# Kernel tuning notes

Hardware: AMD Instinct MI355X
Metric: run time of the kernel (lower is better)

Reference implementation:

```python
import jax, jax.numpy as jnp
import numpy as np

NUM_VERTS = 6890
NUM_FACES = 13776
MAX_COLLISIONS = 8      # BVH(max_collisions=8)
SIGMA = 0.5             # df_cone_height
POINT2PLANE = False
PENALIZE_OUTSIDE = True
COLL_LOSS_WEIGHT = 1.0
EPS = 1e-8


def setup_inputs() -> dict:
    key = jax.random.key(0)
    k1, k2 = jax.random.split(key)
    vertices = jax.random.normal(k1, (1, NUM_VERTS, 3), dtype=jnp.float32)
    # flat face index list, as consumed by index_select(vertices, 1, faces)
    faces = jax.random.randint(k2, (NUM_FACES * 3,), 0, NUM_VERTS, dtype=jnp.int32)
    return {"vertices": vertices, "faces": faces}


def _find_collisions(triangles, faces_mat):
    """Fixed-shape emulation of the BVH broad phase.

    triangles: [B,F,3,3]. Returns collision_idxs [B, F*K, 2] int32 with -1 padding,
    pairs (receiver, intruder) whose AABBs overlap, excluding pairs of triangles
    that share a vertex (as the BVH does; this also removes self-pairs).
    """
    B, F = triangles.shape[0], triangles.shape[1]
    bbmin = triangles.min(axis=2)   # [B,F,3]
    bbmax = triangles.max(axis=2)   # [B,F,3]
    overlap = jnp.ones((B, F, F), dtype=bool)
    for a in range(3):  # fixed 3-axis loop
        lo = bbmin[:, :, a]
        hi = bbmax[:, :, a]
        overlap = overlap & (lo[:, :, None] <= hi[:, None, :]) & (lo[:, None, :] <= hi[:, :, None])
    # triangles sharing any vertex are never reported as collisions
    share = jnp.zeros((F, F), dtype=bool)
    for a in range(3):
        for b in range(3):
            share = share | (faces_mat[:, a][:, None] == faces_mat[:, b][None, :])
    valid = overlap & ~share[None]
    vals, idxs = jax.lax.top_k(valid.astype(jnp.float32), MAX_COLLISIONS)  # [B,F,K]
    intr = jnp.where(vals > 0, idxs, -1)
    recv = jnp.broadcast_to(jnp.arange(F, dtype=jnp.int32)[None, :, None], intr.shape)
    recv = jnp.where(intr >= 0, recv, -1)
    return jnp.stack([recv.reshape(B, -1), intr.reshape(B, -1)], axis=-1)  # [B,F*K,2]


def _cone_field_penalty(src_tri, pts):
    """Conical distance-field penalty (Tzionas et al.) of src triangles
    evaluated at the 3 vertices of the paired triangle.
    src_tri: [B,P,3,3] field-generating triangles; pts: [B,P,3,3] query vertices.
    Returns per-pair penalty [B,P].
    """
    e0 = src_tri[..., 1, :] - src_tri[..., 0, :]
    e1 = src_tri[..., 2, :] - src_tri[..., 0, :]
    n = jnp.cross(e0, e1)
    n = n / (jnp.linalg.norm(n, axis=-1, keepdims=True) + EPS)  # unit normal
    c = src_tri.mean(axis=-2)                                    # triangle center
    u = pts - c[..., None, :]                                    # [B,P,3,3]
    h = jnp.sum(u * n[..., None, :], axis=-1)                    # signed height [B,P,3]
    r = jnp.linalg.norm(u - h[..., None] * n[..., None, :], axis=-1)  # radial dist
    radial = jax.nn.relu(1.0 - r / SIGMA)        # linear falloff of the cone
    depth = jax.nn.relu(-h)                      # penetration depth behind the face
    if PENALIZE_OUTSIDE:
        depth = depth + jax.nn.relu(h) * jnp.exp(-h / SIGMA)  # soft outside penalty
    phi = radial * depth
    per_v = radial * h * h if POINT2PLANE else phi * phi
    return per_v.sum(axis=-1)  # sum over the 3 query vertices -> [B,P]


def reference(vertices, faces):
    B = vertices.shape[0]
    triangles = vertices[:, faces, :].reshape(B, -1, 3, 3)  # [B,F,3,3]
    faces_mat = faces.reshape(-1, 3)
    # collision search runs under no_grad in the original
    coll = _find_collisions(jax.lax.stop_gradient(triangles), faces_mat)  # [B,P,2]
    valid = (coll[..., 0] >= 0)
    recv_idx = jnp.maximum(coll[..., 0], 0)
    intr_idx = jnp.maximum(coll[..., 1], 0)
    bi = jnp.arange(B)[:, None]
    recv_tri = triangles[bi, recv_idx]  # [B,P,3,3]
    intr_tri = triangles[bi, intr_idx]  # [B,P,3,3]
    pen = _cone_field_penalty(recv_tri, intr_tri) + _cone_field_penalty(intr_tri, recv_tri)
    return COLL_LOSS_WEIGHT * jnp.sum(jnp.where(valid, pen, 0.0))
```

## Files before the change

kernel.cpp:

```cpp
#include <hip/hip_runtime.h>

#define NF   13776
#define NFP  13824
#define KMAX 8
#define EPS  1e-8f
#define CBLK 2048

__global__ __launch_bounds__(256) void prep_kernel(
    const float* __restrict__ verts,
    const int*   __restrict__ faces,
    float4* __restrict__ tri,
    float4* __restrict__ lo4, float4* __restrict__ hi4,
    int* __restrict__ f2)
{
    int f = blockIdx.x * blockDim.x + threadIdx.x;
    if (f >= NFP) return;
    if (f >= NF) {
        lo4[f] = make_float4(INFINITY, INFINITY, INFINITY, __int_as_float(-1));
        hi4[f] = make_float4(-INFINITY, -INFINITY, -INFINITY, __int_as_float(-1));
        f2[f]  = -1;
        return;
    }
    int ia = faces[3 * f + 0], ib = faces[3 * f + 1], ic = faces[3 * f + 2];
    float ax = verts[3 * ia + 0], ay = verts[3 * ia + 1], az = verts[3 * ia + 2];
    float bx = verts[3 * ib + 0], by = verts[3 * ib + 1], bz = verts[3 * ib + 2];
    float cx = verts[3 * ic + 0], cy = verts[3 * ic + 1], cz = verts[3 * ic + 2];
    tri[3 * f + 0] = make_float4(ax, ay, az, bx);
    tri[3 * f + 1] = make_float4(by, bz, cx, cy);
    tri[3 * f + 2] = make_float4(cz, 0.f, 0.f, 0.f);
    lo4[f] = make_float4(fminf(ax, fminf(bx, cx)),
                         fminf(ay, fminf(by, cy)),
                         fminf(az, fminf(bz, cz)), __int_as_float(ia));
    hi4[f] = make_float4(fmaxf(ax, fmaxf(bx, cx)),
                         fmaxf(ay, fmaxf(by, cy)),
                         fmaxf(az, fmaxf(bz, cz)), __int_as_float(ib));
    f2[f] = ic;
}

__device__ __forceinline__ float cone_pen_v(const float* s,
                                            float px, float py, float pz) {
    float e0x = s[3] - s[0], e0y = s[4] - s[1], e0z = s[5] - s[2];
    float e1x = s[6] - s[0], e1y = s[7] - s[1], e1z = s[8] - s[2];
    float nx = e0y * e1z - e0z * e1y;
    float ny = e0z * e1x - e0x * e1z;
    float nz = e0x * e1y - e0y * e1x;
    float inv = 1.0f / (sqrtf(nx * nx + ny * ny + nz * nz) + EPS);
    nx *= inv; ny *= inv; nz *= inv;
    const float third = 1.0f / 3.0f;
    float cx = (s[0] + s[3] + s[6]) * third;
    float cy = (s[1] + s[4] + s[7]) * third;
    float cz = (s[2] + s[5] + s[8]) * third;
    float ux = px - cx, uy = py - cy, uz = pz - cz;
    float h = ux * nx + uy * ny + uz * nz;
    float rx = ux - h * nx, ry = uy - h * ny, rz = uz - h * nz;
    float r = sqrtf(rx * rx + ry * ry + rz * rz);
    float radial = fmaxf(0.0f, 1.0f - 2.0f * r);
    float depth = (h < 0.0f) ? -h : h * expf(-2.0f * h);
    float phi = radial * depth;
    return phi * phi;
}

__global__ __launch_bounds__(256) void coll_kernel(
    const float4* __restrict__ tri,
    const float4* __restrict__ lo4, const float4* __restrict__ hi4,
    const int* __restrict__ f2,
    float* __restrict__ partial)
{
    const int lane = threadIdx.x & 63;
    const int wid  = threadIdx.x >> 6;
    const int gw   = (blockIdx.x * blockDim.x + threadIdx.x) >> 6;
    const int nw   = (gridDim.x * blockDim.x) >> 6;

    float acc = 0.0f;

    for (int i = gw; i < NF; i += nw) {
        float4 rlo = lo4[i], rhi = hi4[i];
        int fa0 = __float_as_int(rlo.w);
        int fa1 = __float_as_int(rhi.w);
        int fa2 = f2[i];

        int nc = 0;
        int hj = -1;
        for (int base = 0; base < NFP && nc < KMAX; base += 64) {
            int j = base + lane;
            float4 jlo = lo4[j];
            float4 jhi = hi4[j];
            int jf2 = f2[j];
            bool ov = (rlo.x <= jhi.x) & (jlo.x <= rhi.x)
                    & (rlo.y <= jhi.y) & (jlo.y <= rhi.y)
                    & (rlo.z <= jhi.z) & (jlo.z <= rhi.z);
            int fb0 = __float_as_int(jlo.w);
            int fb1 = __float_as_int(jhi.w);
            bool share = (fb0 == fa0) | (fb0 == fa1) | (fb0 == fa2)
                       | (fb1 == fa0) | (fb1 == fa1) | (fb1 == fa2)
                       | (jf2 == fa0) | (jf2 == fa1) | (jf2 == fa2);
            bool valid = ov & !share;
            unsigned long long mask = __ballot(valid);
            int cnt  = __popcll(mask);
            int take = min(cnt, KMAX - nc);
            if (lane >= nc && lane < nc + take) {
                int t = lane - nc;
                unsigned long long m = mask;
                for (int q = 0; q < t; ++q) m &= (m - 1);
                hj = base + __builtin_ctzll(m);
            }
            nc += take;
        }

        int k = lane >> 3;
        int t = lane & 7;
        int hjk = __shfl(hj, k);
        float p = 0.0f;
        if (t < 6 && k < nc) {
            int d = (t >= 3) ? 1 : 0;
            int v = t - 3 * d;
            int si = d ? hjk : i;
            int qi = d ? i : hjk;
            float4 s0 = tri[3 * si + 0];
            float4 s1 = tri[3 * si + 1];
            float4 s2 = tri[3 * si + 2];
            float s[9] = { s0.x, s0.y, s0.z, s0.w, s1.x, s1.y, s1.z, s1.w, s2.x };
            const float* qp = (const float*)(tri + 3 * qi);
            p = cone_pen_v(s, qp[3 * v + 0], qp[3 * v + 1], qp[3 * v + 2]);
        }
        acc += p;
    }

#pragma unroll
    for (int off = 32; off > 0; off >>= 1) acc += __shfl_xor(acc, off);
    __shared__ float wsum[4];
    if (lane == 0) wsum[wid] = acc;
    __syncthreads();
    if (threadIdx.x == 0)
        partial[blockIdx.x] = wsum[0] + wsum[1] + wsum[2] + wsum[3];
}

__global__ __launch_bounds__(256) void reduce_kernel(
    const float* __restrict__ partial, float* __restrict__ out)
{
    float a = 0.0f;
    for (int idx = threadIdx.x; idx < CBLK; idx += 256) a += partial[idx];
#pragma unroll
    for (int off = 32; off > 0; off >>= 1) a += __shfl_xor(a, off);
    __shared__ float ws[4];
    int lane = threadIdx.x & 63, wid = threadIdx.x >> 6;
    if (lane == 0) ws[wid] = a;
    __syncthreads();
    if (threadIdx.x == 0) out[0] = ws[0] + ws[1] + ws[2] + ws[3];
}

extern "C" void kernel_launch(void* const* d_in, const int* in_sizes, int n_in,
                              void* d_out, int out_size, void* d_ws, size_t ws_size,
                              hipStream_t stream) {
    const float* verts = (const float*)d_in[0];
    const int*   faces = (const int*)d_in[1];
    float* out = (float*)d_out;

    float4* tri = (float4*)d_ws;
    float4* lo4 = tri + NFP * 3;
    float4* hi4 = lo4 + NFP;
    int*    f2  = (int*)(hi4 + NFP);
    float*  partial = (float*)(f2 + NFP);

    prep_kernel<<<NFP / 256, 256, 0, stream>>>(verts, faces, tri, lo4, hi4, f2);
    coll_kernel<<<CBLK, 256, 0, stream>>>(tri, lo4, hi4, f2, partial);
    reduce_kernel<<<1, 256, 0, stream>>>(partial, out);
}
```

Before: 67.84 us.

## Fuse AABB prep into collision kernel and precompute first candidate chunk per lane

```diff
diff --git a/kernel.cpp b/kernel.cpp
--- a/kernel.cpp
+++ b/kernel.cpp
@@ -1,40 +1,28 @@
 #include <hip/hip_runtime.h>
 
+#define NV   6890
 #define NF   13776
-#define NFP  13824
 #define KMAX 8
 #define EPS  1e-8f
-#define CBLK 2048
+#define CBLK 1024
 
-__global__ __launch_bounds__(256) void prep_kernel(
-    const float* __restrict__ verts,
-    const int*   __restrict__ faces,
-    float4* __restrict__ tri,
-    float4* __restrict__ lo4, float4* __restrict__ hi4,
-    int* __restrict__ f2)
+__device__ __forceinline__ void face_aabb(const float* __restrict__ verts,
+                                          const int*   __restrict__ faces,
+                                          int f,
+                                          float& lx, float& ly, float& lz,
+                                          float& hx, float& hy, float& hz,
+                                          int& i0, int& i1, int& i2)
 {
-    int f = blockIdx.x * blockDim.x + threadIdx.x;
-    if (f >= NFP) return;
-    if (f >= NF) {
-        lo4[f] = make_float4(INFINITY, INFINITY, INFINITY, __int_as_float(-1));
-        hi4[f] = make_float4(-INFINITY, -INFINITY, -INFINITY, __int_as_float(-1));
-        f2[f]  = -1;
-        return;
-    }
-    int ia = faces[3 * f + 0], ib = faces[3 * f + 1], ic = faces[3 * f + 2];
-    float ax = verts[3 * ia + 0], ay = verts[3 * ia + 1], az = verts[3 * ia + 2];
-    float bx = verts[3 * ib + 0], by = verts[3 * ib + 1], bz = verts[3 * ib + 2];
-    float cx = verts[3 * ic + 0], cy = verts[3 * ic + 1], cz = verts[3 * ic + 2];
-    tri[3 * f + 0] = make_float4(ax, ay, az, bx);
-    tri[3 * f + 1] = make_float4(by, bz, cx, cy);
-    tri[3 * f + 2] = make_float4(cz, 0.f, 0.f, 0.f);
-    lo4[f] = make_float4(fminf(ax, fminf(bx, cx)),
-                         fminf(ay, fminf(by, cy)),
-                         fminf(az, fminf(bz, cz)), __int_as_float(ia));
-    hi4[f] = make_float4(fmaxf(ax, fmaxf(bx, cx)),
-                         fmaxf(ay, fmaxf(by, cy)),
-                         fmaxf(az, fmaxf(bz, cz)), __int_as_float(ib));
-    f2[f] = ic;
+    i0 = faces[3 * f + 0]; i1 = faces[3 * f + 1]; i2 = faces[3 * f + 2];
+    float ax = verts[3 * i0 + 0], ay = verts[3 * i0 + 1], az = verts[3 * i0 + 2];
+    float bx = verts[3 * i1 + 0], by = verts[3 * i1 + 1], bz = verts[3 * i1 + 2];
+    float cx = verts[3 * i2 + 0], cy = verts[3 * i2 + 1], cz = verts[3 * i2 + 2];
+    lx = fminf(ax, fminf(bx, cx));
+    ly = fminf(ay, fminf(by, cy));
+    lz = fminf(az, fminf(bz, cz));
+    hx = fmaxf(ax, fmaxf(bx, cx));
+    hy = fmaxf(ay, fmaxf(by, cy));
+    hz = fmaxf(az, fmaxf(bz, cz));
 }
 
 __device__ __forceinline__ float cone_pen_v(const float* s,
@@ -61,9 +49,8 @@
 }
 
 __global__ __launch_bounds__(256) void coll_kernel(
-    const float4* __restrict__ tri,
-    const float4* __restrict__ lo4, const float4* __restrict__ hi4,
-    const int* __restrict__ f2,
+    const float* __restrict__ verts,
+    const int*   __restrict__ faces,
     float* __restrict__ partial)
 {
     const int lane = threadIdx.x & 63;
@@ -71,40 +58,66 @@
     const int gw   = (blockIdx.x * blockDim.x + threadIdx.x) >> 6;
     const int nw   = (gridDim.x * blockDim.x) >> 6;
 
+    float c0lx, c0ly, c0lz, c0hx, c0hy, c0hz;
+    int c0a, c0b, c0c;
+    face_aabb(verts, faces, lane, c0lx, c0ly, c0lz, c0hx, c0hy, c0hz,
+              c0a, c0b, c0c);
+
     float acc = 0.0f;
 
     for (int i = gw; i < NF; i += nw) {
-        float4 rlo = lo4[i], rhi = hi4[i];
-        int fa0 = __float_as_int(rlo.w);
-        int fa1 = __float_as_int(rhi.w);
-        int fa2 = f2[i];
+        float rlx, rly, rlz, rhx, rhy, rhz;
+        int fa0, fa1, fa2;
+        face_aabb(verts, faces, i, rlx, rly, rlz, rhx, rhy, rhz,
+                  fa0, fa1, fa2);
 
         int nc = 0;
         int hj = -1;
-        for (int base = 0; base < NFP && nc < KMAX; base += 64) {
-            int j = base + lane;
-            float4 jlo = lo4[j];
-            float4 jhi = hi4[j];
-            int jf2 = f2[j];
-            bool ov = (rlo.x <= jhi.x) & (jlo.x <= rhi.x)
-                    & (rlo.y <= jhi.y) & (jlo.y <= rhi.y)
-                    & (rlo.z <= jhi.z) & (jlo.z <= rhi.z);
-            int fb0 = __float_as_int(jlo.w);
-            int fb1 = __float_as_int(jhi.w);
-            bool share = (fb0 == fa0) | (fb0 == fa1) | (fb0 == fa2)
-                       | (fb1 == fa0) | (fb1 == fa1) | (fb1 == fa2)
-                       | (jf2 == fa0) | (jf2 == fa1) | (jf2 == fa2);
+
+        {
+            bool ov = (rlx <= c0hx) & (c0lx <= rhx)
+                    & (rly <= c0hy) & (c0ly <= rhy)
+                    & (rlz <= c0hz) & (c0lz <= rhz);
+            bool share = (c0a == fa0) | (c0a == fa1) | (c0a == fa2)
+                       | (c0b == fa0) | (c0b == fa1) | (c0b == fa2)
+                       | (c0c == fa0) | (c0c == fa1) | (c0c == fa2);
             bool valid = ov & !share;
             unsigned long long mask = __ballot(valid);
-            int cnt  = __popcll(mask);
-            int take = min(cnt, KMAX - nc);
-            if (lane >= nc && lane < nc + take) {
-                int t = lane - nc;
+            int cnt = __popcll(mask);
+            nc = min(cnt, KMAX);
+            if (lane < nc) {
                 unsigned long long m = mask;
-                for (int q = 0; q < t; ++q) m &= (m - 1);
-                hj = base + __builtin_ctzll(m);
+                for (int q = 0; q < lane; ++q) m &= (m - 1);
+                hj = __builtin_ctzll(m);
             }
-            nc += take;
+        }
+
+        if (nc < KMAX) {
+            for (int base = 64; base < NF && nc < KMAX; base += 64) {
+                int j = base + lane;
+                int jc = min(j, NF - 1);
+                float jlx, jly, jlz, jhx, jhy, jhz;
+                int fb0, fb1, fb2;
+                face_aabb(verts, faces, jc, jlx, jly, jlz, jhx, jhy, jhz,
+                          fb0, fb1, fb2);
+                bool ov = (rlx <= jhx) & (jlx <= rhx)
+                        & (rly <= jhy) & (jly <= rhy)
+                        & (rlz <= jhz) & (jlz <= rhz);
+                bool share = (fb0 == fa0) | (fb0 == fa1) | (fb0 == fa2)
+                           | (fb1 == fa0) | (fb1 == fa1) | (fb1 == fa2)
+                           | (fb2 == fa0) | (fb2 == fa1) | (fb2 == fa2);
+                bool valid = ov & !share & (j < NF);
+                unsigned long long mask = __ballot(valid);
+                int cnt  = __popcll(mask);
+                int take = min(cnt, KMAX - nc);
+                if (take > 0 && lane >= nc && lane < nc + take) {
+                    int t = lane - nc;
+                    unsigned long long m = mask;
+                    for (int q = 0; q < t; ++q) m &= (m - 1);
+                    hj = base + __builtin_ctzll(m);
+                }
+                nc += take;
+            }
         }
 
         int k = lane >> 3;
@@ -116,12 +129,12 @@
             int v = t - 3 * d;
             int si = d ? hjk : i;
             int qi = d ? i : hjk;
-            float4 s0 = tri[3 * si + 0];
-            float4 s1 = tri[3 * si + 1];
-            float4 s2 = tri[3 * si + 2];
-            float s[9] = { s0.x, s0.y, s0.z, s0.w, s1.x, s1.y, s1.z, s1.w, s2.x };
-            const float* qp = (const float*)(tri + 3 * qi);
-            p = cone_pen_v(s, qp[3 * v + 0], qp[3 * v + 1], qp[3 * v + 2]);
+            int sa = faces[3 * si + 0], sb = faces[3 * si + 1], sc = faces[3 * si + 2];
+            float s[9] = { verts[3 * sa + 0], verts[3 * sa + 1], verts[3 * sa + 2],
+                           verts[3 * sb + 0], verts[3 * sb + 1], verts[3 * sb + 2],
+                           verts[3 * sc + 0], verts[3 * sc + 1], verts[3 * sc + 2] };
+            int qv = faces[3 * qi + v];
+            p = cone_pen_v(s, verts[3 * qv + 0], verts[3 * qv + 1], verts[3 * qv + 2]);
         }
         acc += p;
     }
@@ -156,13 +169,8 @@
     const int*   faces = (const int*)d_in[1];
     float* out = (float*)d_out;
 
-    float4* tri = (float4*)d_ws;
-    float4* lo4 = tri + NFP * 3;
-    float4* hi4 = lo4 + NFP;
-    int*    f2  = (int*)(hi4 + NFP);
-    float*  partial = (float*)(f2 + NFP);
+    float* partial = (float*)d_ws;
 
-    prep_kernel<<<NFP / 256, 256, 0, stream>>>(verts, faces, tri, lo4, hi4, f2);
-    coll_kernel<<<CBLK, 256, 0, stream>>>(tri, lo4, hi4, f2, partial);
+    coll_kernel<<<CBLK, 256, 0, stream>>>(verts, faces, partial);
     reduce_kernel<<<1, 256, 0, stream>>>(partial, out);
 }
```

New measurement: 66.66 us. About the same (-1.7%).
